# Kernel tuning notes

Hardware: AMD Instinct MI355X
Metric: run time of the kernel (lower is better)

Reference implementation:

```python
import jax, jax.numpy as jnp
import numpy as np


def setup_inputs() -> dict:
    key = jax.random.key(0)
    ks = jax.random.split(key, 8)
    B, C, H, W = 8, 64, 64, 64
    Cr = C // 8  # ratio=8 reduction, also PAM q/k channels
    return {
        "x": jax.random.normal(ks[0], (B, C, H, W), dtype=jnp.float32),
        "fc1_w": jax.random.normal(ks[1], (Cr, C), dtype=jnp.float32) * 0.1,
        "fc2_w": jax.random.normal(ks[2], (C, Cr), dtype=jnp.float32) * 0.1,
        "q_w": jax.random.normal(ks[3], (Cr, C), dtype=jnp.float32) * 0.1,
        "q_b": jnp.zeros((Cr,), dtype=jnp.float32),
        "k_w": jax.random.normal(ks[4], (Cr, C), dtype=jnp.float32) * 0.1,
        "k_b": jnp.zeros((Cr,), dtype=jnp.float32),
        "v_w": jax.random.normal(ks[5], (C, C), dtype=jnp.float32) * 0.1,
        "v_b": jnp.zeros((C,), dtype=jnp.float32),
        "gamma": jnp.zeros((1,), dtype=jnp.float32),
        "sa_w": jax.random.normal(ks[6], (1, 2, 7, 7), dtype=jnp.float32) * 0.1,
    }


def _pcbam(x, fc1_w, fc2_w, q_w, q_b, k_w, k_b, v_w, v_b, gamma, sa_w):
    B, C, H, W = x.shape
    N = H * W

    # --- Channel attention (CBAM channel branch) ---
    avg = jnp.mean(x, axis=(2, 3))          # [B,C]
    mx = jnp.max(x, axis=(2, 3))            # [B,C]
    def mlp(v):
        h = jax.nn.relu(jnp.einsum('bc,rc->br', v, fc1_w))
        return jnp.einsum('br,cr->bc', h, fc2_w)
    ca = jax.nn.sigmoid(mlp(avg) + mlp(mx))  # [B,C]
    x_c = x * ca[:, :, None, None]

    # --- Spatial attention ---
    avg_s = jnp.mean(x_c, axis=1, keepdims=True)  # [B,1,H,W]
    max_s = jnp.max(x_c, axis=1, keepdims=True)   # [B,1,H,W]
    sa_in = jnp.concatenate([avg_s, max_s], axis=1)  # [B,2,H,W]
    sa_out = jax.lax.conv_general_dilated(
        sa_in, sa_w, window_strides=(1, 1), padding=((3, 3), (3, 3)),
        dimension_numbers=('NCHW', 'OIHW', 'NCHW'))  # [B,1,H,W]
    x_s = x_c * jax.nn.sigmoid(sa_out)

    # --- Position attention (PAM), on original x ---
    q = jnp.einsum('bchw,rc->brhw', x, q_w) + q_b[None, :, None, None]
    k = jnp.einsum('bchw,rc->brhw', x, k_w) + k_b[None, :, None, None]
    v = jnp.einsum('bchw,oc->bohw', x, v_w) + v_b[None, :, None, None]
    q = q.reshape(B, -1, N)  # [B,Cr,N]
    k = k.reshape(B, -1, N)
    v = v.reshape(B, C, N)
    # energy[b,i,j] = sum_r q[b,r,i] * k[b,r,j]; softmax over j
    energy = jnp.einsum('bri,brj->bij', q, k)
    attn = jax.nn.softmax(energy, axis=-1)
    # out[b,c,i] = sum_j v[b,c,j] * attn[b,i,j]
    pam = jnp.einsum('bcj,bij->bci', v, attn).reshape(B, C, H, W)
    x_p = gamma[0] * pam + x

    return x_s + x_p


def reference(x, fc1_w, fc2_w, q_w, q_b, k_w, k_b, v_w, v_b, gamma, sa_w):
    return _pcbam(x, fc1_w, fc2_w, q_w, q_b, k_w, k_b, v_w, v_b, gamma, sa_w)
```

## Files before the change

### kernel.cpp

```cpp
#include <hip/hip_runtime.h>
#include <math.h>

#define B 8
#define C 64
#define HH 64
#define WW 64
#define N 4096
#define CR 8

typedef __attribute__((ext_vector_type(8))) short short8;
typedef __attribute__((ext_vector_type(4))) float f32x4;

__device__ __forceinline__ float sigmoidf_(float x) { return 1.0f / (1.0f + __expf(-x)); }

__device__ __forceinline__ unsigned int bfr_(float x) {
    return (__float_as_uint(x) + 0x8000u) >> 16;
}

__global__ __launch_bounds__(256) void k_reduce_bc(const float* __restrict__ x,
                                                   float* __restrict__ avg,
                                                   float* __restrict__ mx) {
    int bc = blockIdx.x;
    const float4* xp = (const float4*)(x + (size_t)bc * N);
    float s = 0.f, m = -INFINITY;
    for (int i = threadIdx.x; i < N / 4; i += 256) {
        float4 v = xp[i];
        s += v.x + v.y + v.z + v.w;
        m = fmaxf(m, fmaxf(fmaxf(v.x, v.y), fmaxf(v.z, v.w)));
    }
    for (int off = 32; off; off >>= 1) {
        s += __shfl_down(s, off);
        m = fmaxf(m, __shfl_down(m, off));
    }
    __shared__ float ls[4], lm[4];
    int wave = threadIdx.x >> 6;
    if ((threadIdx.x & 63) == 0) { ls[wave] = s; lm[wave] = m; }
    __syncthreads();
    if (threadIdx.x == 0) {
        float S = ls[0] + ls[1] + ls[2] + ls[3];
        float M = fmaxf(fmaxf(lm[0], lm[1]), fmaxf(lm[2], lm[3]));
        avg[bc] = S / (float)N;
        mx[bc] = M;
    }
}

__global__ __launch_bounds__(64) void k_ca(const float* __restrict__ avg,
                                           const float* __restrict__ mx,
                                           const float* __restrict__ fc1,
                                           const float* __restrict__ fc2,
                                           float* __restrict__ ca) {
    int b = blockIdx.x;
    int t = threadIdx.x;
    __shared__ float sa[C], sm[C], h[2 * CR];
    sa[t] = avg[b * C + t];
    sm[t] = mx[b * C + t];
    __syncthreads();
    if (t < 2 * CR) {
        int r = t & 7;
        const float* src = (t < CR) ? sa : sm;
        float acc = 0.f;
        for (int c2 = 0; c2 < C; c2++) acc += src[c2] * fc1[r * C + c2];
        h[t] = fmaxf(acc, 0.f);
    }
    __syncthreads();
    float acc = 0.f;
    #pragma unroll
    for (int r = 0; r < CR; r++) acc += (h[r] + h[CR + r]) * fc2[t * CR + r];
    ca[b * C + t] = sigmoidf_(acc);
}

__global__ __launch_bounds__(256) void k_spatial_stats(const float* __restrict__ x,
                                                       const float* __restrict__ ca,
                                                       float* __restrict__ avg_s,
                                                       float* __restrict__ max_s) {
    int b = blockIdx.x >> 4;
    int hw = (blockIdx.x & 15) * 256 + threadIdx.x;
    __shared__ float lca[C];
    if (threadIdx.x < C) lca[threadIdx.x] = ca[b * C + threadIdx.x];
    __syncthreads();
    const float* xb = x + (size_t)b * C * N + hw;
    float s = 0.f, m = -INFINITY;
    #pragma unroll
    for (int c = 0; c < C; c++) {
        float v = xb[(size_t)c * N] * lca[c];
        s += v;
        m = fmaxf(m, v);
    }
    avg_s[b * N + hw] = s / (float)C;
    max_s[b * N + hw] = m;
}

__global__ __launch_bounds__(256) void k_conv_sa(const float* __restrict__ avg_s,
                                                 const float* __restrict__ max_s,
                                                 const float* __restrict__ w,
                                                 float* __restrict__ ssig) {
    __shared__ float lw[98];
    if (threadIdx.x < 98) lw[threadIdx.x] = w[threadIdx.x];
    __syncthreads();
    int b = blockIdx.x >> 4;
    int hw = (blockIdx.x & 15) * 256 + threadIdx.x;
    int h = hw >> 6, wc = hw & 63;
    const float* A = avg_s + b * N;
    const float* M = max_s + b * N;
    float acc = 0.f;
    for (int ky = 0; ky < 7; ky++) {
        int ih = h + ky - 3;
        if (ih < 0 || ih >= HH) continue;
        for (int kx = 0; kx < 7; kx++) {
            int iw = wc + kx - 3;
            if (iw < 0 || iw >= WW) continue;
            int idx = ih * WW + iw;
            acc += A[idx] * lw[ky * 7 + kx] + M[idx] * lw[49 + ky * 7 + kx];
        }
    }
    ssig[b * N + hw] = sigmoidf_(acc);
}

__global__ __launch_bounds__(256) void k_qkv(const float* __restrict__ x,
                                             const float* __restrict__ qw, const float* __restrict__ qb,
                                             const float* __restrict__ kw, const float* __restrict__ kb,
                                             const float* __restrict__ vw, const float* __restrict__ vb,
                                             const float* __restrict__ gamma,
                                             unsigned short* __restrict__ qT,
                                             unsigned short* __restrict__ kT,
                                             unsigned short* __restrict__ vbf) {
    if (gamma[0] == 0.f) return;
    __shared__ float xl[C][64];
    __shared__ float vwt[C][68];
    __shared__ float qwl[CR * C], kwl[CR * C];
    int b = blockIdx.y;
    int p0 = blockIdx.x * 64;
    int t = threadIdx.x;
    for (int idx = t; idx < C * 64; idx += 256) {
        int c2 = idx >> 6, pix = idx & 63;
        xl[c2][pix] = x[((size_t)b * C + c2) * N + p0 + pix];
    }
    for (int idx = t; idx < C * C; idx += 256) {
        int co = idx >> 6, ci = idx & 63;
        vwt[ci][co] = vw[idx];
    }
    for (int idx = t; idx < CR * C; idx += 256) {
        qwl[idx] = qw[idx];
        kwl[idx] = kw[idx];
    }
    __syncthreads();
    int pix = t & 63, quarter = t >> 6;
    float accv[16];
    #pragma unroll
    for (int i = 0; i < 16; i++) accv[i] = 0.f;
    float accq0 = 0.f, accq1 = 0.f, acck0 = 0.f, acck1 = 0.f;
    for (int ci = 0; ci < C; ci++) {
        float xv = xl[ci][pix];
        accq0 += qwl[(quarter * 2 + 0) * C + ci] * xv;
        accq1 += qwl[(quarter * 2 + 1) * C + ci] * xv;
        acck0 += kwl[(quarter * 2 + 0) * C + ci] * xv;
        acck1 += kwl[(quarter * 2 + 1) * C + ci] * xv;
        const float4* row = (const float4*)&vwt[ci][quarter * 16];
        #pragma unroll
        for (int m2 = 0; m2 < 4; m2++) {
            float4 w4 = row[m2];
            accv[m2 * 4 + 0] += w4.x * xv;
            accv[m2 * 4 + 1] += w4.y * xv;
            accv[m2 * 4 + 2] += w4.z * xv;
            accv[m2 * 4 + 3] += w4.w * xv;
        }
    }
    int pg = p0 + pix;
    int r0 = quarter * 2;
    unsigned int qpk = bfr_(accq0 + qb[r0]) | (bfr_(accq1 + qb[r0 + 1]) << 16);
    unsigned int kpk = bfr_(acck0 + kb[r0]) | (bfr_(acck1 + kb[r0 + 1]) << 16);
    *(unsigned int*)(qT + ((size_t)b * N + pg) * 8 + r0) = qpk;
    *(unsigned int*)(kT + ((size_t)b * N + pg) * 8 + r0) = kpk;
    #pragma unroll
    for (int i = 0; i < 16; i++) {
        int co = quarter * 16 + i;
        vbf[((size_t)b * C + co) * N + pg] = (unsigned short)bfr_(accv[i] + vb[co]);
    }
}

template <int S>
__global__ __launch_bounds__(256, 2) void k_flash_mfma(
    const unsigned short* __restrict__ qT,
    const unsigned short* __restrict__ kT,
    const unsigned short* __restrict__ vbf,
    const float* __restrict__ gamma,
    float* __restrict__ pA, float* __restrict__ pM, float* __restrict__ pL) {
    if (gamma[0] == 0.f) return;
    __shared__ unsigned short p_lds[4][32 * 64];
    const int b = blockIdx.y, p = blockIdx.z;
    const int tid = threadIdx.x;
    const int w = tid >> 6, lane = tid & 63;
    const int l16 = lane & 15, grp = lane >> 4;
    const int i0 = blockIdx.x * 128 + w * 32;
    char* pbase = (char*)&p_lds[w][0];
    const int swz = (l16 & 7) << 4;

    short8 qf[2];
    #pragma unroll
    for (int ifr = 0; ifr < 2; ifr++) {
        qf[ifr] = short8{};
        if (grp == 0) qf[ifr] = *(const short8*)(qT + ((size_t)b * N + i0 + ifr * 16 + l16) * 8);
    }

    f32x4 acc[2][4];
    #pragma unroll
    for (int ifr = 0; ifr < 2; ifr++)
        #pragma unroll
        for (int cf = 0; cf < 4; cf++) acc[ifr][cf] = f32x4{0.f, 0.f, 0.f, 0.f};
    float m[2] = {-INFINITY, -INFINITY}, l[2] = {0.f, 0.f};

    const int L = N / S;
    const int T = L / 64;
    const int jbase = p * L;
    const unsigned short* vbase = vbf + (size_t)b * C * N;
    const unsigned short* kbase = kT + (size_t)b * N * 8;

    short8 kf[2][4];
    #pragma unroll
    for (int ss = 0; ss < 2; ss++)
        #pragma unroll
        for (int jf = 0; jf < 4; jf++) kf[ss][jf] = short8{};
    #pragma unroll
    for (int jf = 0; jf < 4; jf++) {
        if (grp == 0) kf[0][jf] = *(const short8*)(kbase + (size_t)(jbase + jf * 16 + l16) * 8);
    }

    #pragma unroll 2
    for (int t = 0; t < T; t++) {
        const int cur = t & 1, nxt = cur ^ 1;
        const int j0 = jbase + t * 64;
        short8 vf[2][4];
        #pragma unroll
        for (int h = 0; h < 2; h++)
            #pragma unroll
            for (int cf = 0; cf < 4; cf++)
                vf[h][cf] = *(const short8*)(vbase + (size_t)(cf * 16 + l16) * N + j0 + h * 32 + grp * 8);
        if (t + 1 < T) {
            #pragma unroll
            for (int jf = 0; jf < 4; jf++) {
                if (grp == 0) kf[nxt][jf] = *(const short8*)(kbase + (size_t)(j0 + 64 + jf * 16 + l16) * 8);
            }
        }
        #pragma unroll
        for (int ifr = 0; ifr < 2; ifr++) {
            f32x4 e[4];
            #pragma unroll
            for (int jf = 0; jf < 4; jf++)
                e[jf] = __builtin_amdgcn_mfma_f32_16x16x32_bf16(kf[cur][jf], qf[ifr],
                                                                f32x4{0.f, 0.f, 0.f, 0.f}, 0, 0, 0);
            float tmax = -INFINITY;
            #pragma unroll
            for (int jf = 0; jf < 4; jf++)
                tmax = fmaxf(tmax, fmaxf(fmaxf(e[jf][0], e[jf][1]), fmaxf(e[jf][2], e[jf][3])));
            tmax = fmaxf(tmax, __shfl_xor(tmax, 16));
            tmax = fmaxf(tmax, __shfl_xor(tmax, 32));
            float mnew = fmaxf(m[ifr], tmax);
            float scale = __expf(m[ifr] - mnew);
            float ladd = 0.f;
            unsigned int pk[8];
            #pragma unroll
            for (int jf = 0; jf < 4; jf++) {
                float p0 = __expf(e[jf][0] - mnew);
                float p1 = __expf(e[jf][1] - mnew);
                float p2 = __expf(e[jf][2] - mnew);
                float p3 = __expf(e[jf][3] - mnew);
                ladd += (p0 + p1) + (p2 + p3);
                pk[jf * 2 + 0] = bfr_(p0) | (bfr_(p1) << 16);
                pk[jf * 2 + 1] = bfr_(p2) | (bfr_(p3) << 16);
            }
            ladd += __shfl_xor(ladd, 16);
            ladd += __shfl_xor(ladd, 32);
            l[ifr] = l[ifr] * scale + ladd;
            m[ifr] = mnew;
            #pragma unroll
            for (int cf = 0; cf < 4; cf++) {
                acc[ifr][cf][0] *= scale; acc[ifr][cf][1] *= scale;
                acc[ifr][cf][2] *= scale; acc[ifr][cf][3] *= scale;
            }
            const int rowoff = (ifr * 16 + l16) * 128;
            #pragma unroll
            for (int jf = 0; jf < 4; jf++) {
                int j = jf * 16 + grp * 4;
                *(unsigned int*)(pbase + ((rowoff + (j + 0) * 2) ^ swz)) = pk[jf * 2 + 0];
                *(unsigned int*)(pbase + ((rowoff + (j + 2) * 2) ^ swz)) = pk[jf * 2 + 1];
            }
        }
        #pragma unroll
        for (int ifr = 0; ifr < 2; ifr++) {
            const int rowoff = (ifr * 16 + l16) * 128;
            #pragma unroll
            for (int h = 0; h < 2; h++) {
                short8 pf = *(const short8*)(pbase + ((rowoff + (h * 32 + grp * 8) * 2) ^ swz));
                #pragma unroll
                for (int cf = 0; cf < 4; cf++)
                    acc[ifr][cf] = __builtin_amdgcn_mfma_f32_16x16x32_bf16(vf[h][cf], pf, acc[ifr][cf], 0, 0, 0);
            }
        }
    }
    const size_t plane = (size_t)(b * S + p);
    #pragma unroll
    for (int ifr = 0; ifr < 2; ifr++) {
        const int iglob = i0 + ifr * 16 + l16;
        #pragma unroll
        for (int cf = 0; cf < 4; cf++)
            #pragma unroll
            for (int r = 0; r < 4; r++)
                pA[(plane * C + cf * 16 + grp * 4 + r) * N + iglob] = acc[ifr][cf][r];
        if (grp == 0) {
            pM[plane * N + iglob] = m[ifr];
            pL[plane * N + iglob] = l[ifr];
        }
    }
}

template <int S>
__global__ __launch_bounds__(256) void k_combine(const float* __restrict__ pA,
                                                 const float* __restrict__ pM,
                                                 const float* __restrict__ pL,
                                                 const float* __restrict__ x,
                                                 const float* __restrict__ ca,
                                                 const float* __restrict__ ssig,
                                                 const float* __restrict__ gamma,
                                                 float* __restrict__ out) {
    int b = blockIdx.y;
    int i = blockIdx.x * 256 + threadIdx.x;
    __shared__ float lca[C];
    if (threadIdx.x < C) lca[threadIdx.x] = ca[b * C + threadIdx.x];
    __syncthreads();
    float g = gamma[0];
    float sg = ssig[b * N + i];
    if (g == 0.f) {
        for (int c = 0; c < C; c++) {
            size_t off = ((size_t)b * C + c) * N + i;
            out[off] = x[off] * (1.f + lca[c] * sg);
        }
        return;
    }
    float mm[S];
    float M = -INFINITY;
    #pragma unroll
    for (int p2 = 0; p2 < S; p2++) {
        mm[p2] = pM[(size_t)(b * S + p2) * N + i];
        M = fmaxf(M, mm[p2]);
    }
    float w[S];
    float lt = 0.f;
    #pragma unroll
    for (int p2 = 0; p2 < S; p2++) {
        w[p2] = __expf(mm[p2] - M);
        lt += w[p2] * pL[(size_t)(b * S + p2) * N + i];
    }
    float inv = 1.0f / lt;
    for (int c = 0; c < C; c++) {
        float a = 0.f;
        #pragma unroll
        for (int p2 = 0; p2 < S; p2++)
            a += w[p2] * pA[((size_t)(b * S + p2) * C + c) * N + i];
        float pam = a * inv;
        size_t off = ((size_t)b * C + c) * N + i;
        out[off] = x[off] * (1.f + lca[c] * sg) + g * pam;
    }
}

extern "C" void kernel_launch(void* const* d_in, const int* in_sizes, int n_in,
                              void* d_out, int out_size, void* d_ws, size_t ws_size,
                              hipStream_t stream) {
    (void)in_sizes; (void)n_in; (void)out_size;
    const float* x   = (const float*)d_in[0];
    const float* fc1 = (const float*)d_in[1];
    const float* fc2 = (const float*)d_in[2];
    const float* qw  = (const float*)d_in[3];
    const float* qb  = (const float*)d_in[4];
    const float* kw  = (const float*)d_in[5];
    const float* kb  = (const float*)d_in[6];
    const float* vw  = (const float*)d_in[7];
    const float* vb  = (const float*)d_in[8];
    const float* gamma = (const float*)d_in[9];
    const float* saw = (const float*)d_in[10];
    float* out = (float*)d_out;
    float* ws = (float*)d_ws;

    float* avg   = ws;
    float* mx    = ws + 512;
    float* ca    = ws + 1024;
    float* avg_s = ws + 2048;
    float* max_s = avg_s + (size_t)B * N;
    float* ssig  = max_s + (size_t)B * N;
    unsigned short* qT  = (unsigned short*)(ssig + (size_t)B * N);
    unsigned short* kT  = qT + (size_t)B * N * 8;
    unsigned short* vbf = kT + (size_t)B * N * 8;
    float* pA = (float*)(vbf + (size_t)B * C * N);

    size_t fixed_bytes = (size_t)((char*)pA - (char*)ws);
    int S = 4;
    if (fixed_bytes + (size_t)B * 4 * N * (C + 2) * 4 > ws_size) S = 2;
    if (fixed_bytes + (size_t)B * 2 * N * (C + 2) * 4 > ws_size) S = 1;
    float* pM = pA + (size_t)B * S * C * N;
    float* pL = pM + (size_t)B * S * N;

    k_reduce_bc<<<B * C, 256, 0, stream>>>(x, avg, mx);
    k_ca<<<B, 64, 0, stream>>>(avg, mx, fc1, fc2, ca);
    k_spatial_stats<<<B * (N / 256), 256, 0, stream>>>(x, ca, avg_s, max_s);
    k_conv_sa<<<B * (N / 256), 256, 0, stream>>>(avg_s, max_s, saw, ssig);
    k_qkv<<<dim3(N / 64, B), 256, 0, stream>>>(x, qw, qb, kw, kb, vw, vb, gamma, qT, kT, vbf);
    if (S == 4) {
        k_flash_mfma<4><<<dim3(N / 128, B, 4), 256, 0, stream>>>(qT, kT, vbf, gamma, pA, pM, pL);
        k_combine<4><<<dim3(N / 256, B), 256, 0, stream>>>(pA, pM, pL, x, ca, ssig, gamma, out);
    } else if (S == 2) {
        k_flash_mfma<2><<<dim3(N / 128, B, 2), 256, 0, stream>>>(qT, kT, vbf, gamma, pA, pM, pL);
        k_combine<2><<<dim3(N / 256, B), 256, 0, stream>>>(pA, pM, pL, x, ca, ssig, gamma, out);
    } else {
        k_flash_mfma<1><<<dim3(N / 128, B, 1), 256, 0, stream>>>(qT, kT, vbf, gamma, pA, pM, pL);
        k_combine<1><<<dim3(N / 256, B), 256, 0, stream>>>(pA, pM, pL, x, ca, ssig, gamma, out);
    }
}
```

Measured before the change: 102.8 us.

## Fuse attention prologue kernels into qkv, flash and output launches

```diff
diff --git a/kernel.cpp b/kernel.cpp
--- a/kernel.cpp
+++ b/kernel.cpp
@@ -17,120 +17,66 @@
     return (__float_as_uint(x) + 0x8000u) >> 16;
 }
 
-__global__ __launch_bounds__(256) void k_reduce_bc(const float* __restrict__ x,
-                                                   float* __restrict__ avg,
-                                                   float* __restrict__ mx) {
-    int bc = blockIdx.x;
-    const float4* xp = (const float4*)(x + (size_t)bc * N);
-    float s = 0.f, m = -INFINITY;
-    for (int i = threadIdx.x; i < N / 4; i += 256) {
-        float4 v = xp[i];
-        s += v.x + v.y + v.z + v.w;
-        m = fmaxf(m, fmaxf(fmaxf(v.x, v.y), fmaxf(v.z, v.w)));
-    }
-    for (int off = 32; off; off >>= 1) {
-        s += __shfl_down(s, off);
-        m = fmaxf(m, __shfl_down(m, off));
-    }
-    __shared__ float ls[4], lm[4];
-    int wave = threadIdx.x >> 6;
-    if ((threadIdx.x & 63) == 0) { ls[wave] = s; lm[wave] = m; }
-    __syncthreads();
-    if (threadIdx.x == 0) {
-        float S = ls[0] + ls[1] + ls[2] + ls[3];
-        float M = fmaxf(fmaxf(lm[0], lm[1]), fmaxf(lm[2], lm[3]));
-        avg[bc] = S / (float)N;
-        mx[bc] = M;
-    }
-}
-
-__global__ __launch_bounds__(64) void k_ca(const float* __restrict__ avg,
-                                           const float* __restrict__ mx,
-                                           const float* __restrict__ fc1,
-                                           const float* __restrict__ fc2,
-                                           float* __restrict__ ca) {
-    int b = blockIdx.x;
+__device__ __forceinline__ void compute_ca_(const float* __restrict__ avg,
+                                            const float* __restrict__ mx,
+                                            const float* __restrict__ fc1,
+                                            const float* __restrict__ fc2,
+                                            int b, float* lca, float* lh) {
     int t = threadIdx.x;
-    __shared__ float sa[C], sm[C], h[2 * CR];
-    sa[t] = avg[b * C + t];
-    sm[t] = mx[b * C + t];
-    __syncthreads();
-    if (t < 2 * CR) {
+    if (t < 16) {
         int r = t & 7;
-        const float* src = (t < CR) ? sa : sm;
+        const float* src = (t < 8) ? (avg + b * C) : (mx + b * C);
         float acc = 0.f;
         for (int c2 = 0; c2 < C; c2++) acc += src[c2] * fc1[r * C + c2];
-        h[t] = fmaxf(acc, 0.f);
+        lh[t] = fmaxf(acc, 0.f);
     }
     __syncthreads();
-    float acc = 0.f;
-    #pragma unroll
-    for (int r = 0; r < CR; r++) acc += (h[r] + h[CR + r]) * fc2[t * CR + r];
-    ca[b * C + t] = sigmoidf_(acc);
-}
-
-__global__ __launch_bounds__(256) void k_spatial_stats(const float* __restrict__ x,
-                                                       const float* __restrict__ ca,
-                                                       float* __restrict__ avg_s,
-                                                       float* __restrict__ max_s) {
-    int b = blockIdx.x >> 4;
-    int hw = (blockIdx.x & 15) * 256 + threadIdx.x;
-    __shared__ float lca[C];
-    if (threadIdx.x < C) lca[threadIdx.x] = ca[b * C + threadIdx.x];
+    if (t < C) {
+        float acc = 0.f;
+        #pragma unroll
+        for (int r = 0; r < CR; r++) acc += (lh[r] + lh[CR + r]) * fc2[t * CR + r];
+        lca[t] = sigmoidf_(acc);
+    }
     __syncthreads();
-    const float* xb = x + (size_t)b * C * N + hw;
-    float s = 0.f, m = -INFINITY;
-    #pragma unroll
-    for (int c = 0; c < C; c++) {
-        float v = xb[(size_t)c * N] * lca[c];
-        s += v;
-        m = fmaxf(m, v);
-    }
-    avg_s[b * N + hw] = s / (float)C;
-    max_s[b * N + hw] = m;
-}
-
-__global__ __launch_bounds__(256) void k_conv_sa(const float* __restrict__ avg_s,
-                                                 const float* __restrict__ max_s,
-                                                 const float* __restrict__ w,
-                                                 float* __restrict__ ssig) {
-    __shared__ float lw[98];
-    if (threadIdx.x < 98) lw[threadIdx.x] = w[threadIdx.x];
-    __syncthreads();
-    int b = blockIdx.x >> 4;
-    int hw = (blockIdx.x & 15) * 256 + threadIdx.x;
-    int h = hw >> 6, wc = hw & 63;
-    const float* A = avg_s + b * N;
-    const float* M = max_s + b * N;
-    float acc = 0.f;
-    for (int ky = 0; ky < 7; ky++) {
-        int ih = h + ky - 3;
-        if (ih < 0 || ih >= HH) continue;
-        for (int kx = 0; kx < 7; kx++) {
-            int iw = wc + kx - 3;
-            if (iw < 0 || iw >= WW) continue;
-            int idx = ih * WW + iw;
-            acc += A[idx] * lw[ky * 7 + kx] + M[idx] * lw[49 + ky * 7 + kx];
-        }
-    }
-    ssig[b * N + hw] = sigmoidf_(acc);
-}
-
-__global__ __launch_bounds__(256) void k_qkv(const float* __restrict__ x,
-                                             const float* __restrict__ qw, const float* __restrict__ qb,
-                                             const float* __restrict__ kw, const float* __restrict__ kb,
-                                             const float* __restrict__ vw, const float* __restrict__ vb,
-                                             const float* __restrict__ gamma,
-                                             unsigned short* __restrict__ qT,
-                                             unsigned short* __restrict__ kT,
-                                             unsigned short* __restrict__ vbf) {
+}
+
+__global__ __launch_bounds__(256) void k_red_qkv(const float* __restrict__ x,
+                                                 const float* __restrict__ qw, const float* __restrict__ qb,
+                                                 const float* __restrict__ kw, const float* __restrict__ kb,
+                                                 const float* __restrict__ vw, const float* __restrict__ vb,
+                                                 const float* __restrict__ gamma,
+                                                 float* __restrict__ avg, float* __restrict__ mx,
+                                                 unsigned short* __restrict__ qT,
+                                                 unsigned short* __restrict__ kT,
+                                                 unsigned short* __restrict__ vbf) {
+    const int b = blockIdx.y, cx = blockIdx.x;
+    const int t = threadIdx.x;
+    {
+        const float4* xp = (const float4*)(x + ((size_t)b * C + cx) * N);
+        float s = 0.f, m = -INFINITY;
+        for (int i = t; i < N / 4; i += 256) {
+            float4 v = xp[i];
+            s += v.x + v.y + v.z + v.w;
+            m = fmaxf(m, fmaxf(fmaxf(v.x, v.y), fmaxf(v.z, v.w)));
+        }
+        for (int off = 32; off; off >>= 1) {
+            s += __shfl_down(s, off);
+            m = fmaxf(m, __shfl_down(m, off));
+        }
+        __shared__ float ls[4], lm[4];
+        int wave = t >> 6;
+        if ((t & 63) == 0) { ls[wave] = s; lm[wave] = m; }
+        __syncthreads();
+        if (t == 0) {
+            avg[b * C + cx] = (ls[0] + ls[1] + ls[2] + ls[3]) / (float)N;
+            mx[b * C + cx] = fmaxf(fmaxf(lm[0], lm[1]), fmaxf(lm[2], lm[3]));
+        }
+    }
     if (gamma[0] == 0.f) return;
     __shared__ float xl[C][64];
     __shared__ float vwt[C][68];
     __shared__ float qwl[CR * C], kwl[CR * C];
-    int b = blockIdx.y;
-    int p0 = blockIdx.x * 64;
-    int t = threadIdx.x;
+    const int p0 = cx * 64;
     for (int idx = t; idx < C * 64; idx += 256) {
         int c2 = idx >> 6, pix = idx & 63;
         xl[c2][pix] = x[((size_t)b * C + c2) * N + p0 + pix];
@@ -179,16 +125,39 @@
 }
 
 template <int S>
-__global__ __launch_bounds__(256, 2) void k_flash_mfma(
+__global__ __launch_bounds__(256, 2) void k_stats_flash(
+    const float* __restrict__ x,
+    const float* __restrict__ avg, const float* __restrict__ mx,
+    const float* __restrict__ fc1, const float* __restrict__ fc2,
+    const float* __restrict__ gamma,
     const unsigned short* __restrict__ qT,
     const unsigned short* __restrict__ kT,
     const unsigned short* __restrict__ vbf,
-    const float* __restrict__ gamma,
+    float* __restrict__ avg_s, float* __restrict__ max_s,
     float* __restrict__ pA, float* __restrict__ pM, float* __restrict__ pL) {
-    if (gamma[0] == 0.f) return;
     __shared__ unsigned short p_lds[4][32 * 64];
+    __shared__ float lca[C], lh[16];
     const int b = blockIdx.y, p = blockIdx.z;
     const int tid = threadIdx.x;
+    if (p == 0) {
+        compute_ca_(avg, mx, fc1, fc2, b, lca, lh);
+        int pix = blockIdx.x * 128 + (tid >> 1);
+        int half = tid & 1;
+        const float* xb = x + (size_t)b * C * N + pix;
+        float s = 0.f, m = -INFINITY;
+        for (int c = half * 32; c < half * 32 + 32; c++) {
+            float v = xb[(size_t)c * N] * lca[c];
+            s += v;
+            m = fmaxf(m, v);
+        }
+        s += __shfl_xor(s, 1);
+        m = fmaxf(m, __shfl_xor(m, 1));
+        if (half == 0) {
+            avg_s[b * N + pix] = s / (float)C;
+            max_s[b * N + pix] = m;
+        }
+    }
+    if (gamma[0] == 0.f) return;
     const int w = tid >> 6, lane = tid & 63;
     const int l16 = lane & 15, grp = lane >> 4;
     const int i0 = blockIdx.x * 128 + w * 32;
@@ -201,7 +170,6 @@
         qf[ifr] = short8{};
         if (grp == 0) qf[ifr] = *(const short8*)(qT + ((size_t)b * N + i0 + ifr * 16 + l16) * 8);
     }
-
     f32x4 acc[2][4];
     #pragma unroll
     for (int ifr = 0; ifr < 2; ifr++)
@@ -314,21 +282,51 @@
 }
 
 template <int S>
-__global__ __launch_bounds__(256) void k_combine(const float* __restrict__ pA,
-                                                 const float* __restrict__ pM,
-                                                 const float* __restrict__ pL,
-                                                 const float* __restrict__ x,
-                                                 const float* __restrict__ ca,
-                                                 const float* __restrict__ ssig,
-                                                 const float* __restrict__ gamma,
-                                                 float* __restrict__ out) {
-    int b = blockIdx.y;
-    int i = blockIdx.x * 256 + threadIdx.x;
-    __shared__ float lca[C];
-    if (threadIdx.x < C) lca[threadIdx.x] = ca[b * C + threadIdx.x];
+__global__ __launch_bounds__(256) void k_out(const float* __restrict__ x,
+                                             const float* __restrict__ avg, const float* __restrict__ mx,
+                                             const float* __restrict__ fc1, const float* __restrict__ fc2,
+                                             const float* __restrict__ avg_s, const float* __restrict__ max_s,
+                                             const float* __restrict__ saw,
+                                             const float* __restrict__ gamma,
+                                             const float* __restrict__ pA, const float* __restrict__ pM,
+                                             const float* __restrict__ pL,
+                                             float* __restrict__ out) {
+    const int b = blockIdx.y;
+    const int i0 = blockIdx.x * 256;
+    const int t = threadIdx.x;
+    __shared__ float lca[C], lh[16], lw[98];
+    __shared__ float sA[10 * 64], sM[10 * 64];
+    if (t < 98) lw[t] = saw[t];
+    compute_ca_(avg, mx, fc1, fc2, b, lca, lh);
+    const int h0 = i0 >> 6;
+    for (int idx = t; idx < 10 * 64; idx += 256) {
+        int r = idx >> 6, wcol = idx & 63;
+        int hh = h0 - 3 + r;
+        float a = 0.f, mm2 = 0.f;
+        if (hh >= 0 && hh < HH) {
+            a = avg_s[b * N + hh * WW + wcol];
+            mm2 = max_s[b * N + hh * WW + wcol];
+        }
+        sA[idx] = a;
+        sM[idx] = mm2;
+    }
     __syncthreads();
-    float g = gamma[0];
-    float sg = ssig[b * N + i];
+    const int lr = (t >> 6) + 3;
+    const int wc = t & 63;
+    float acc = 0.f;
+    #pragma unroll
+    for (int ky = 0; ky < 7; ky++) {
+        #pragma unroll
+        for (int kx = 0; kx < 7; kx++) {
+            int ww = wc + kx - 3;
+            if (ww < 0 || ww >= WW) continue;
+            int idx = (lr + ky - 3) * 64 + ww;
+            acc += sA[idx] * lw[ky * 7 + kx] + sM[idx] * lw[49 + ky * 7 + kx];
+        }
+    }
+    const float sg = sigmoidf_(acc);
+    const int i = i0 + t;
+    const float g = gamma[0];
     if (g == 0.f) {
         for (int c = 0; c < C; c++) {
             size_t off = ((size_t)b * C + c) * N + i;
@@ -382,11 +380,9 @@
 
     float* avg   = ws;
     float* mx    = ws + 512;
-    float* ca    = ws + 1024;
-    float* avg_s = ws + 2048;
+    float* avg_s = ws + 1024;
     float* max_s = avg_s + (size_t)B * N;
-    float* ssig  = max_s + (size_t)B * N;
-    unsigned short* qT  = (unsigned short*)(ssig + (size_t)B * N);
+    unsigned short* qT  = (unsigned short*)(max_s + (size_t)B * N);
     unsigned short* kT  = qT + (size_t)B * N * 8;
     unsigned short* vbf = kT + (size_t)B * N * 8;
     float* pA = (float*)(vbf + (size_t)B * C * N);
@@ -398,19 +394,22 @@
     float* pM = pA + (size_t)B * S * C * N;
     float* pL = pM + (size_t)B * S * N;
 
-    k_reduce_bc<<<B * C, 256, 0, stream>>>(x, avg, mx);
-    k_ca<<<B, 64, 0, stream>>>(avg, mx, fc1, fc2, ca);
-    k_spatial_stats<<<B * (N / 256), 256, 0, stream>>>(x, ca, avg_s, max_s);
-    k_conv_sa<<<B * (N / 256), 256, 0, stream>>>(avg_s, max_s, saw, ssig);
-    k_qkv<<<dim3(N / 64, B), 256, 0, stream>>>(x, qw, qb, kw, kb, vw, vb, gamma, qT, kT, vbf);
+    k_red_qkv<<<dim3(C, B), 256, 0, stream>>>(x, qw, qb, kw, kb, vw, vb, gamma,
+                                              avg, mx, qT, kT, vbf);
     if (S == 4) {
-        k_flash_mfma<4><<<dim3(N / 128, B, 4), 256, 0, stream>>>(qT, kT, vbf, gamma, pA, pM, pL);
-        k_combine<4><<<dim3(N / 256, B), 256, 0, stream>>>(pA, pM, pL, x, ca, ssig, gamma, out);
+        k_stats_flash<4><<<dim3(N / 128, B, 4), 256, 0, stream>>>(
+            x, avg, mx, fc1, fc2, gamma, qT, kT, vbf, avg_s, max_s, pA, pM, pL);
+        k_out<4><<<dim3(N / 256, B), 256, 0, stream>>>(
+            x, avg, mx, fc1, fc2, avg_s, max_s, saw, gamma, pA, pM, pL, out);
     } else if (S == 2) {
-        k_flash_mfma<2><<<dim3(N / 128, B, 2), 256, 0, stream>>>(qT, kT, vbf, gamma, pA, pM, pL);
-        k_combine<2><<<dim3(N / 256, B), 256, 0, stream>>>(pA, pM, pL, x, ca, ssig, gamma, out);
+        k_stats_flash<2><<<dim3(N / 128, B, 2), 256, 0, stream>>>(
+            x, avg, mx, fc1, fc2, gamma, qT, kT, vbf, avg_s, max_s, pA, pM, pL);
+        k_out<2><<<dim3(N / 256, B), 256, 0, stream>>>(
+            x, avg, mx, fc1, fc2, avg_s, max_s, saw, gamma, pA, pM, pL, out);
     } else {
-        k_flash_mfma<1><<<dim3(N / 128, B, 1), 256, 0, stream>>>(qT, kT, vbf, gamma, pA, pM, pL);
-        k_combine<1><<<dim3(N / 256, B), 256, 0, stream>>>(pA, pM, pL, x, ca, ssig, gamma, out);
-    }
-}
+        k_stats_flash<1><<<dim3(N / 128, B, 1), 256, 0, stream>>>(
+            x, avg, mx, fc1, fc2, gamma, qT, kT, vbf, avg_s, max_s, pA, pM, pL);
+        k_out<1><<<dim3(N / 256, B), 256, 0, stream>>>(
+            x, avg, mx, fc1, fc2, avg_s, max_s, saw, gamma, pA, pM, pL, out);
+    }
+}
```

Result: faster. 96.97 us, median of 2 (-5.6%).
